# Performance work log

Hardware: AMD Instinct MI355X
Metric: run time of the kernel (lower is better)

The kernel has to match this reference:

```python
import math
import jax, jax.numpy as jnp
import numpy as np

NUM_BINS = 128
NUM_FREQS = 64
HEAD_DIM = 2 * NUM_FREQS
NUM_QUERIES = 16384
EPS = 1e-8


def setup_inputs() -> dict:
    key = jax.random.key(0)
    k1, k2 = jax.random.split(key, 2)
    Q = jax.random.normal(k1, (NUM_QUERIES, HEAD_DIM), dtype=jnp.float32)
    rotated_probes = jax.random.normal(k2, (NUM_BINS, HEAD_DIM), dtype=jnp.float32)
    # probes are expected pre-normalized
    rotated_probes = rotated_probes / (jnp.linalg.norm(rotated_probes, axis=-1, keepdims=True) + EPS)
    init_value = math.log(math.e - 1.0)  # softplus(init)=1
    q_weights_raw = jnp.full((NUM_BINS, NUM_FREQS), init_value, dtype=jnp.float32)
    q_magnitude_weights = jnp.zeros((NUM_BINS, NUM_FREQS), dtype=jnp.float32)
    q_bias = jnp.zeros((NUM_BINS,), dtype=jnp.float32)
    return {
        "Q": Q,
        "rotated_probes": rotated_probes,
        "q_weights_raw": q_weights_raw,
        "q_magnitude_weights": q_magnitude_weights,
        "q_bias": q_bias,
    }


def reference(Q, rotated_probes, q_weights_raw, q_magnitude_weights, q_bias):
    F = NUM_FREQS
    # L2 normalize Q
    norm = jnp.linalg.norm(Q, axis=-1, keepdims=True)
    Qn = Q / (norm + EPS)
    Q_real, Q_imag = Qn[:, :F], Qn[:, F:]            # (Nq, F)
    P_real, P_imag = rotated_probes[:, :F], rotated_probes[:, F:]  # (B, F)
    # broadcast per-frequency complex error and distance: (Nq, B, F)
    err_r = P_real[None, :, :] - Q_real[:, None, :]
    err_i = P_imag[None, :, :] - Q_imag[:, None, :]
    distance = jnp.sqrt(err_r * err_r + err_i * err_i + EPS)
    # magnitude features on normalized Q: (Nq, F)
    Q_mag = jnp.sqrt(Q_real * Q_real + Q_imag * Q_imag + EPS)
    eff_w = -jax.nn.softplus(q_weights_raw)          # (B, F), negative weights
    distance_term = jnp.einsum('qbf,bf->qb', distance, eff_w)
    magnitude_term = Q_mag @ q_magnitude_weights.T   # (Nq, B)
    return distance_term + magnitude_term + q_bias[None, :]
```

## Files before the change

### kernel.cpp

```cpp
#include <hip/hip_runtime.h>

#define NBINS 128
#define NFREQ 64
#define HDIM 128
#define NQ 16384
#define EPSF 1e-8f

#define PT_OFF 0
#define QR_OFF (128 * 1024)
#define PLANE_BYTES ((size_t)NQ * NFREQ * 4)
#define QI_OFF (QR_OFF + PLANE_BYTES)
#define QM_OFF (QI_OFF + PLANE_BYTES)
#define WS_NEEDED (QM_OFF + PLANE_BYTES)

#define QN_BLOCKS (NQ / 64)
#define PACK_BLOCKS ((NBINS * NFREQ + 255) / 256)

__global__ __launch_bounds__(256) void prologue6(
    const float* __restrict__ Q,
    const float* __restrict__ probes,
    const float* __restrict__ wraw,
    const float* __restrict__ mw,
    float4* __restrict__ probeT,
    float* __restrict__ QR, float* __restrict__ QI, float* __restrict__ QM) {
  const int blk = blockIdx.x;
  const int t = threadIdx.x;
  if (blk < QN_BLOCKS) {
    const int l = t & 3;
    const int q = blk * 64 + (t >> 2);
    const float* qp = Q + (size_t)q * HDIM;
    float re[16], im[16];
    #pragma unroll
    for (int k = 0; k < 4; ++k) {
      *reinterpret_cast<float4*>(&re[k * 4]) =
          *reinterpret_cast<const float4*>(qp + 16 * l + k * 4);
      *reinterpret_cast<float4*>(&im[k * 4]) =
          *reinterpret_cast<const float4*>(qp + NFREQ + 16 * l + k * 4);
    }
    float s = 0.0f;
    #pragma unroll
    for (int k = 0; k < 16; ++k) {
      s = fmaf(re[k], re[k], s);
      s = fmaf(im[k], im[k], s);
    }
    s += __shfl_xor(s, 1, 4);
    s += __shfl_xor(s, 2, 4);
    const float inv = 1.0f / (__builtin_amdgcn_sqrtf(s) + EPSF);
    #pragma unroll
    for (int k = 0; k < 16; ++k) {
      const int f = 16 * l + k;
      const float qr = re[k] * inv;
      const float qi = im[k] * inv;
      const float qm = __builtin_amdgcn_sqrtf(fmaf(qr, qr, fmaf(qi, qi, EPSF)));
      QR[(size_t)f * NQ + q] = qr;
      QI[(size_t)f * NQ + q] = qi;
      QM[(size_t)f * NQ + q] = qm;
    }
  } else {
    const int idx = (blk - QN_BLOCKS) * 256 + t;
    if (idx >= NBINS * NFREQ) return;
    const int b = idx >> 6;
    const int f = idx & 63;
    const float pr = probes[b * HDIM + f];
    const float pi = probes[b * HDIM + NFREQ + f];
    const float x = wraw[b * NFREQ + f];
    const float sp = fmaxf(x, 0.0f) + log1pf(expf(-fabsf(x)));
    const float m = mw[b * NFREQ + f];
    const int tIdx = (b >> 4) * 8 + (f >> 3);
    probeT[tIdx * 128 + (b & 15) * 8 + (f & 7)] = make_float4(pr, pi, -sp, m);
  }
}

__global__ __launch_bounds__(512) void scorer6(
    const float4* __restrict__ probeT,
    const float* __restrict__ QR, const float* __restrict__ QI,
    const float* __restrict__ QM,
    const float* __restrict__ bias,
    float* __restrict__ out) {
  __shared__ float part[8][16][64];
  const int t = threadIdx.x;
  const int lane = t & 63;
  const int fq = __builtin_amdgcn_readfirstlane(t >> 6);
  const int qc = blockIdx.x >> 3;
  const int bq = blockIdx.x & 7;
  const int q = qc * 64 + lane;

  float qr[8], qi[8], qm[8];
  #pragma unroll
  for (int j = 0; j < 8; ++j) {
    const size_t fo = (size_t)(fq * 8 + j) * NQ + q;
    qr[j] = QR[fo];
    qi[j] = QI[fo];
    qm[j] = QM[fo];
  }

  const float4* tile = probeT + (bq * 8 + fq) * 128;

  #pragma unroll 4
  for (int bi = 0; bi < 16; ++bi) {
    float a = 0.0f;
    #pragma unroll
    for (int j = 0; j < 8; ++j) {
      const float4 c = tile[bi * 8 + j];
      float er = c.x - qr[j];
      float ei = c.y - qi[j];
      float d2 = fmaf(er, er, EPSF);
      d2 = fmaf(ei, ei, d2);
      float d = __builtin_amdgcn_sqrtf(d2);
      a = fmaf(d, c.z, a);
      a = fmaf(qm[j], c.w, a);
    }
    part[fq][bi][lane] = a;
  }
  __syncthreads();

  const int qe = t >> 3;
  const int k = t & 7;
  float s0 = 0.0f, s1 = 0.0f;
  #pragma unroll
  for (int w = 0; w < 8; ++w) {
    s0 += part[w][2 * k][qe];
    s1 += part[w][2 * k + 1][qe];
  }
  const int bb = bq * 16 + 2 * k;
  float2 o = make_float2(s0 + bias[bb], s1 + bias[bb + 1]);
  *reinterpret_cast<float2*>(&out[(size_t)(qc * 64 + qe) * NBINS + bb]) = o;
}

__global__ __launch_bounds__(256) void pack_fb(
    const float* __restrict__ probes,
    const float* __restrict__ wraw,
    const float* __restrict__ mw,
    float4* __restrict__ packed) {
  int idx = blockIdx.x * 256 + threadIdx.x;
  if (idx >= NBINS * NFREQ) return;
  int b = idx >> 6;
  int f = idx & 63;
  float pr = probes[b * HDIM + f];
  float pi = probes[b * HDIM + NFREQ + f];
  float x = wraw[b * NFREQ + f];
  float sp = fmaxf(x, 0.0f) + log1pf(expf(-fabsf(x)));
  packed[f * NBINS + b] = make_float4(pr, pi, -sp, mw[b * NFREQ + f]);
}

__global__ __launch_bounds__(256) void scorer_fallback(
    const float* __restrict__ Q,
    const float4* __restrict__ packed,
    const float* __restrict__ bias,
    float* __restrict__ out) {
  __shared__ float4 qlds[32][64];
  const int t = threadIdx.x;
  const int qbase = blockIdx.x * 32;
  {
    const int qi = t >> 3;
    const int f0 = (t & 7) * 8;
    const float* qp = Q + (size_t)(qbase + qi) * HDIM;
    float4 r0 = *reinterpret_cast<const float4*>(qp + f0);
    float4 r1 = *reinterpret_cast<const float4*>(qp + f0 + 4);
    float4 i0 = *reinterpret_cast<const float4*>(qp + NFREQ + f0);
    float4 i1 = *reinterpret_cast<const float4*>(qp + NFREQ + f0 + 4);
    float s = r0.x*r0.x + r0.y*r0.y + r0.z*r0.z + r0.w*r0.w
            + r1.x*r1.x + r1.y*r1.y + r1.z*r1.z + r1.w*r1.w
            + i0.x*i0.x + i0.y*i0.y + i0.z*i0.z + i0.w*i0.w
            + i1.x*i1.x + i1.y*i1.y + i1.z*i1.z + i1.w*i1.w;
    s += __shfl_xor(s, 1, 8);
    s += __shfl_xor(s, 2, 8);
    s += __shfl_xor(s, 4, 8);
    float inv = 1.0f / (__builtin_amdgcn_sqrtf(s) + EPSF);
    float re[8] = {r0.x, r0.y, r0.z, r0.w, r1.x, r1.y, r1.z, r1.w};
    float im[8] = {i0.x, i0.y, i0.z, i0.w, i1.x, i1.y, i1.z, i1.w};
    #pragma unroll
    for (int j = 0; j < 8; ++j) {
      float qr = re[j] * inv;
      float qim = im[j] * inv;
      float qm = __builtin_amdgcn_sqrtf(fmaf(qr, qr, fmaf(qim, qim, EPSF)));
      qlds[qi][f0 + j] = make_float4(qr, qim, qm, 0.0f);
    }
  }
  __syncthreads();
  const int w = t >> 6;
  const int lane = t & 63;
  const int b = (w & 1) * 64 + lane;
  const int qoff = (w >> 1) * 16;
  const float bb = bias[b];
  float acc[16];
  #pragma unroll
  for (int q = 0; q < 16; ++q) acc[q] = 0.0f;
  #pragma unroll
  for (int fc = 0; fc < 4; ++fc) {
    float4 c[16];
    #pragma unroll
    for (int fi = 0; fi < 16; ++fi)
      c[fi] = packed[(fc * 16 + fi) * NBINS + b];
    #pragma unroll 4
    for (int fi = 0; fi < 16; ++fi) {
      #pragma unroll
      for (int q = 0; q < 16; ++q) {
        float4 qv = qlds[qoff + q][fc * 16 + fi];
        float er = c[fi].x - qv.x;
        float ei = c[fi].y - qv.y;
        float d2 = fmaf(er, er, EPSF);
        d2 = fmaf(ei, ei, d2);
        float d = __builtin_amdgcn_sqrtf(d2);
        acc[q] = fmaf(d, c[fi].z, acc[q]);
        acc[q] = fmaf(qv.z, c[fi].w, acc[q]);
      }
    }
  }
  #pragma unroll
  for (int q = 0; q < 16; ++q)
    out[(size_t)(qbase + qoff + q) * NBINS + b] = acc[q] + bb;
}

extern "C" void kernel_launch(void* const* d_in, const int* in_sizes, int n_in,
                              void* d_out, int out_size, void* d_ws, size_t ws_size,
                              hipStream_t stream) {
  const float* Q      = (const float*)d_in[0];
  const float* probes = (const float*)d_in[1];
  const float* wraw   = (const float*)d_in[2];
  const float* mw     = (const float*)d_in[3];
  const float* bias   = (const float*)d_in[4];
  float* out = (float*)d_out;

  if (ws_size >= WS_NEEDED) {
    float4* probeT = (float4*)((char*)d_ws + PT_OFF);
    float* QRp = (float*)((char*)d_ws + QR_OFF);
    float* QIp = (float*)((char*)d_ws + QI_OFF);
    float* QMp = (float*)((char*)d_ws + QM_OFF);
    prologue6<<<QN_BLOCKS + PACK_BLOCKS, 256, 0, stream>>>(
        Q, probes, wraw, mw, probeT, QRp, QIp, QMp);
    scorer6<<<256 * 8, 512, 0, stream>>>(probeT, QRp, QIp, QMp, bias, out);
  } else {
    float4* packed = (float4*)d_ws;
    pack_fb<<<PACK_BLOCKS, 256, 0, stream>>>(probes, wraw, mw, packed);
    scorer_fallback<<<NQ / 32, 256, 0, stream>>>(Q, packed, bias, out);
  }
}
```

Before: 45.50 us.

## Restructure scorer with bins-per-lane, LDS query tiles and packed FP32 math

Replaces the frequency-split scorer, which needed an LDS cross-wave reduction, with a design where each lane owns two bins and four queries. Queries are staged in LDS from a new per-query interleaved layout holding negated real and imaginary parts plus magnitudes. Probe data is split into four planes read with float4 loads. The inner math uses v_pk_add/v_pk_fma packed FP32 instructions to halve the VALU instruction count around the sqrt. This removes the partial-sum LDS traffic and the strided plane reads. The cost is larger per-query global reads of probe data per block and reliance on inline asm for packed ops.

```diff
diff --git a/kernel.cpp b/kernel.cpp
--- a/kernel.cpp
+++ b/kernel.cpp
@@ -6,23 +6,34 @@
 #define NQ 16384
 #define EPSF 1e-8f
 
-#define PT_OFF 0
-#define QR_OFF (128 * 1024)
-#define PLANE_BYTES ((size_t)NQ * NFREQ * 4)
-#define QI_OFF (QR_OFF + PLANE_BYTES)
-#define QM_OFF (QI_OFF + PLANE_BYTES)
-#define WS_NEEDED (QM_OFF + PLANE_BYTES)
+typedef float v2f __attribute__((ext_vector_type(2)));
+
+__device__ __forceinline__ v2f pk_add(v2f a, v2f b) {
+  v2f r;
+  asm("v_pk_add_f32 %0, %1, %2" : "=v"(r) : "v"(a), "v"(b));
+  return r;
+}
+__device__ __forceinline__ v2f pk_fma(v2f a, v2f b, v2f c) {
+  v2f r;
+  asm("v_pk_fma_f32 %0, %1, %2, %3" : "=v"(r) : "v"(a), "v"(b), "v"(c));
+  return r;
+}
+
+#define PLANE_FLOATS (NBINS * NFREQ)
+#define QB_OFF (128 * 1024)
+#define QB_STRIDE 192
+#define WS_NEEDED ((size_t)QB_OFF + (size_t)NQ * QB_STRIDE * 4)
 
 #define QN_BLOCKS (NQ / 64)
 #define PACK_BLOCKS ((NBINS * NFREQ + 255) / 256)
 
-__global__ __launch_bounds__(256) void prologue6(
+__global__ __launch_bounds__(256) void prologue7(
     const float* __restrict__ Q,
     const float* __restrict__ probes,
     const float* __restrict__ wraw,
     const float* __restrict__ mw,
-    float4* __restrict__ probeT,
-    float* __restrict__ QR, float* __restrict__ QI, float* __restrict__ QM) {
+    float* __restrict__ planes,
+    float* __restrict__ Qb) {
   const int blk = blockIdx.x;
   const int t = threadIdx.x;
   if (blk < QN_BLOCKS) {
@@ -46,15 +57,23 @@
     s += __shfl_xor(s, 1, 4);
     s += __shfl_xor(s, 2, 4);
     const float inv = 1.0f / (__builtin_amdgcn_sqrtf(s) + EPSF);
-    #pragma unroll
-    for (int k = 0; k < 16; ++k) {
-      const int f = 16 * l + k;
-      const float qr = re[k] * inv;
-      const float qi = im[k] * inv;
-      const float qm = __builtin_amdgcn_sqrtf(fmaf(qr, qr, fmaf(qi, qi, EPSF)));
-      QR[(size_t)f * NQ + q] = qr;
-      QI[(size_t)f * NQ + q] = qi;
-      QM[(size_t)f * NQ + q] = qm;
+    float4* qb4 = reinterpret_cast<float4*>(Qb + (size_t)q * QB_STRIDE);
+    #pragma unroll
+    for (int cc = 0; cc < 4; ++cc) {
+      const int fc = 4 * l + cc;
+      float nqr[4], nqi[4], qm[4];
+      #pragma unroll
+      for (int j = 0; j < 4; ++j) {
+        const int k = cc * 4 + j;
+        const float qr = re[k] * inv;
+        const float qi = im[k] * inv;
+        nqr[j] = -qr;
+        nqi[j] = -qi;
+        qm[j] = __builtin_amdgcn_sqrtf(fmaf(qr, qr, fmaf(qi, qi, EPSF)));
+      }
+      qb4[fc * 3 + 0] = make_float4(nqr[0], nqr[1], nqr[2], nqr[3]);
+      qb4[fc * 3 + 1] = make_float4(nqi[0], nqi[1], nqi[2], nqi[3]);
+      qb4[fc * 3 + 2] = make_float4(qm[0], qm[1], qm[2], qm[3]);
     }
   } else {
     const int idx = (blk - QN_BLOCKS) * 256 + t;
@@ -66,65 +85,103 @@
     const float x = wraw[b * NFREQ + f];
     const float sp = fmaxf(x, 0.0f) + log1pf(expf(-fabsf(x)));
     const float m = mw[b * NFREQ + f];
-    const int tIdx = (b >> 4) * 8 + (f >> 3);
-    probeT[tIdx * 128 + (b & 15) * 8 + (f & 7)] = make_float4(pr, pi, -sp, m);
-  }
-}
-
-__global__ __launch_bounds__(512) void scorer6(
-    const float4* __restrict__ probeT,
-    const float* __restrict__ QR, const float* __restrict__ QI,
-    const float* __restrict__ QM,
+    const int fc = f >> 2, bc = b >> 6, b0 = b & 63, fo = f & 3;
+    const size_t e = (size_t)(((fc * 2 + bc) * 64 + b0) * 4 + fo);
+    planes[0 * PLANE_FLOATS + e] = pr;
+    planes[1 * PLANE_FLOATS + e] = pi;
+    planes[2 * PLANE_FLOATS + e] = -sp;
+    planes[3 * PLANE_FLOATS + e] = m;
+  }
+}
+
+__device__ __forceinline__ v2f dstep(v2f cpr, v2f cpi, v2f cw, v2f cmw,
+                                     v2f nqr, v2f nqi, v2f qm, v2f eps2, v2f acc) {
+  v2f er = pk_add(cpr, nqr);
+  v2f ei = pk_add(cpi, nqi);
+  v2f d2 = pk_fma(er, er, eps2);
+  d2 = pk_fma(ei, ei, d2);
+  v2f d;
+  d.x = __builtin_amdgcn_sqrtf(d2.x);
+  d.y = __builtin_amdgcn_sqrtf(d2.y);
+  acc = pk_fma(d, cw, acc);
+  acc = pk_fma(qm, cmw, acc);
+  return acc;
+}
+
+__global__ __launch_bounds__(256) void scorer7(
+    const float* __restrict__ planes,
+    const float* __restrict__ Qb,
     const float* __restrict__ bias,
     float* __restrict__ out) {
-  __shared__ float part[8][16][64];
+  __shared__ float4 qlds4[768];
   const int t = threadIdx.x;
-  const int lane = t & 63;
-  const int fq = __builtin_amdgcn_readfirstlane(t >> 6);
-  const int qc = blockIdx.x >> 3;
-  const int bq = blockIdx.x & 7;
-  const int q = qc * 64 + lane;
-
-  float qr[8], qi[8], qm[8];
-  #pragma unroll
-  for (int j = 0; j < 8; ++j) {
-    const size_t fo = (size_t)(fq * 8 + j) * NQ + q;
-    qr[j] = QR[fo];
-    qi[j] = QI[fo];
-    qm[j] = QM[fo];
-  }
-
-  const float4* tile = probeT + (bq * 8 + fq) * 128;
-
-  #pragma unroll 4
-  for (int bi = 0; bi < 16; ++bi) {
-    float a = 0.0f;
-    #pragma unroll
-    for (int j = 0; j < 8; ++j) {
-      const float4 c = tile[bi * 8 + j];
-      float er = c.x - qr[j];
-      float ei = c.y - qi[j];
-      float d2 = fmaf(er, er, EPSF);
-      d2 = fmaf(ei, ei, d2);
-      float d = __builtin_amdgcn_sqrtf(d2);
-      a = fmaf(d, c.z, a);
-      a = fmaf(qm[j], c.w, a);
-    }
-    part[fq][bi][lane] = a;
+  const int qblk = blockIdx.x * 16;
+
+  {
+    const float4* src = reinterpret_cast<const float4*>(Qb + (size_t)qblk * QB_STRIDE);
+    qlds4[t] = src[t];
+    qlds4[t + 256] = src[t + 256];
+    qlds4[t + 512] = src[t + 512];
   }
   __syncthreads();
 
-  const int qe = t >> 3;
-  const int k = t & 7;
-  float s0 = 0.0f, s1 = 0.0f;
-  #pragma unroll
-  for (int w = 0; w < 8; ++w) {
-    s0 += part[w][2 * k][qe];
-    s1 += part[w][2 * k + 1][qe];
-  }
-  const int bb = bq * 16 + 2 * k;
-  float2 o = make_float2(s0 + bias[bb], s1 + bias[bb + 1]);
-  *reinterpret_cast<float2*>(&out[(size_t)(qc * 64 + qe) * NBINS + bb]) = o;
+  const int b0 = t & 63;
+  const int w = __builtin_amdgcn_readfirstlane(t >> 6);
+  const int q0 = w * 4;
+
+  const float4* PR = reinterpret_cast<const float4*>(planes + 0 * PLANE_FLOATS);
+  const float4* PI = reinterpret_cast<const float4*>(planes + 1 * PLANE_FLOATS);
+  const float4* PW = reinterpret_cast<const float4*>(planes + 2 * PLANE_FLOATS);
+  const float4* PM = reinterpret_cast<const float4*>(planes + 3 * PLANE_FLOATS);
+
+  const v2f eps2 = {EPSF, EPSF};
+  v2f acc[4][2];
+  #pragma unroll
+  for (int q = 0; q < 4; ++q) {
+    acc[q][0] = (v2f){0.0f, 0.0f};
+    acc[q][1] = (v2f){0.0f, 0.0f};
+  }
+
+  #pragma unroll 1
+  for (int fc = 0; fc < 16; ++fc) {
+    const int pb = fc * 128 + b0;
+    const float4 pr0 = PR[pb], pr1 = PR[pb + 64];
+    const float4 pi0 = PI[pb], pi1 = PI[pb + 64];
+    const float4 w0  = PW[pb], w1  = PW[pb + 64];
+    const float4 m0  = PM[pb], m1  = PM[pb + 64];
+    const v2f pr0a = {pr0.x, pr0.y}, pr0b = {pr0.z, pr0.w};
+    const v2f pr1a = {pr1.x, pr1.y}, pr1b = {pr1.z, pr1.w};
+    const v2f pi0a = {pi0.x, pi0.y}, pi0b = {pi0.z, pi0.w};
+    const v2f pi1a = {pi1.x, pi1.y}, pi1b = {pi1.z, pi1.w};
+    const v2f w0a = {w0.x, w0.y}, w0b = {w0.z, w0.w};
+    const v2f w1a = {w1.x, w1.y}, w1b = {w1.z, w1.w};
+    const v2f m0a = {m0.x, m0.y}, m0b = {m0.z, m0.w};
+    const v2f m1a = {m1.x, m1.y}, m1b = {m1.z, m1.w};
+
+    #pragma unroll
+    for (int q = 0; q < 4; ++q) {
+      const int qb = ((q0 + q) * 16 + fc) * 3;
+      const float4 a0 = qlds4[qb + 0];
+      const float4 a1 = qlds4[qb + 1];
+      const float4 a2 = qlds4[qb + 2];
+      const v2f nqr_a = {a0.x, a0.y}, nqr_b = {a0.z, a0.w};
+      const v2f nqi_a = {a1.x, a1.y}, nqi_b = {a1.z, a1.w};
+      const v2f qm_a = {a2.x, a2.y}, qm_b = {a2.z, a2.w};
+      acc[q][0] = dstep(pr0a, pi0a, w0a, m0a, nqr_a, nqi_a, qm_a, eps2, acc[q][0]);
+      acc[q][0] = dstep(pr0b, pi0b, w0b, m0b, nqr_b, nqi_b, qm_b, eps2, acc[q][0]);
+      acc[q][1] = dstep(pr1a, pi1a, w1a, m1a, nqr_a, nqi_a, qm_a, eps2, acc[q][1]);
+      acc[q][1] = dstep(pr1b, pi1b, w1b, m1b, nqr_b, nqi_b, qm_b, eps2, acc[q][1]);
+    }
+  }
+
+  const float bias0 = bias[b0];
+  const float bias1 = bias[64 + b0];
+  #pragma unroll
+  for (int q = 0; q < 4; ++q) {
+    const size_t row = (size_t)(qblk + q0 + q) * NBINS;
+    out[row + b0]      = acc[q][0].x + acc[q][0].y + bias0;
+    out[row + 64 + b0] = acc[q][1].x + acc[q][1].y + bias1;
+  }
 }
 
 __global__ __launch_bounds__(256) void pack_fb(
@@ -223,13 +280,11 @@
   float* out = (float*)d_out;
 
   if (ws_size >= WS_NEEDED) {
-    float4* probeT = (float4*)((char*)d_ws + PT_OFF);
-    float* QRp = (float*)((char*)d_ws + QR_OFF);
-    float* QIp = (float*)((char*)d_ws + QI_OFF);
-    float* QMp = (float*)((char*)d_ws + QM_OFF);
-    prologue6<<<QN_BLOCKS + PACK_BLOCKS, 256, 0, stream>>>(
-        Q, probes, wraw, mw, probeT, QRp, QIp, QMp);
-    scorer6<<<256 * 8, 512, 0, stream>>>(probeT, QRp, QIp, QMp, bias, out);
+    float* planes = (float*)d_ws;
+    float* Qb = (float*)((char*)d_ws + QB_OFF);
+    prologue7<<<QN_BLOCKS + PACK_BLOCKS, 256, 0, stream>>>(
+        Q, probes, wraw, mw, planes, Qb);
+    scorer7<<<NQ / 16, 256, 0, stream>>>(planes, Qb, bias, out);
   } else {
     float4* packed = (float4*)d_ws;
     pack_fb<<<PACK_BLOCKS, 256, 0, stream>>>(probes, wraw, mw, packed);
```

Result: faster. 40.63 us (-10.7%).
